# Optimization experiments

Measured on AMD Instinct MI355X. Metric: run time of the kernel, lower is better.

Reference implementation:

```python
import jax, jax.numpy as jnp
import numpy as np

B, S, E, H, V, C = 256, 20, 512, 512, 32000, 1000


def _lstm_step(x, h, c, W, U, b):
    # Keras LSTM, activation='relu', recurrent_activation='sigmoid', gate order i,f,c,o
    z = x @ W + h @ U + b  # (B, 4H)
    i, f, g, o = jnp.split(z, 4, axis=-1)
    i = jax.nn.sigmoid(i)
    f = jax.nn.sigmoid(f)
    g = jax.nn.relu(g)
    o = jax.nn.sigmoid(o)
    c_new = f * c + i * g
    h_new = o * jax.nn.relu(c_new)
    return h_new, c_new


def setup_inputs() -> dict:
    key = jax.random.key(0)
    ks = jax.random.split(key, 24)
    std = 0.05
    d_in1 = S * E + 2 * E  # flattened encoder output + word embed + speaker embed
    inp = {
        "encoded_output": jax.random.normal(ks[0], (B, S, E), jnp.float32),
        "word_embedding": jax.random.normal(ks[1], (B, E), jnp.float32),
        "h0": jax.random.normal(ks[2], (B, H), jnp.float32) * std,
        "c0": jax.random.normal(ks[3], (B, H), jnp.float32) * std,
        "speaker": jax.random.randint(ks[4], (B,), 0, C),
        "addressee": jax.random.randint(ks[5], (B,), 0, C),
        "persona_emb": jax.random.normal(ks[6], (C, E), jnp.float32) * 0.1,
        "W1": jax.random.normal(ks[7], (d_in1, 4 * H), jnp.float32) * std,
        "U1": jax.random.normal(ks[8], (H, 4 * H), jnp.float32) * std,
        "b1": jnp.zeros((4 * H,), jnp.float32),
        "W2": jax.random.normal(ks[9], (H, 4 * H), jnp.float32) * std,
        "U2": jax.random.normal(ks[10], (H, 4 * H), jnp.float32) * std,
        "b2": jnp.zeros((4 * H,), jnp.float32),
        "W3": jax.random.normal(ks[11], (H, 4 * H), jnp.float32) * std,
        "U3": jax.random.normal(ks[12], (H, 4 * H), jnp.float32) * std,
        "b3": jnp.zeros((4 * H,), jnp.float32),
        "W4": jax.random.normal(ks[13], (H, 4 * H), jnp.float32) * std,
        "U4": jax.random.normal(ks[14], (H, 4 * H), jnp.float32) * std,
        "b4": jnp.zeros((4 * H,), jnp.float32),
        "Wd": jax.random.normal(ks[15], (H, V), jnp.float32) * std,
        "bd": jnp.zeros((V,), jnp.float32),
    }
    return inp


def reference(encoded_output, word_embedding, h0, c0, speaker, addressee,
              persona_emb, W1, U1, b1, W2, U2, b2, W3, U3, b3, W4, U4, b4, Wd, bd):
    b = encoded_output.shape[0]
    # The Python double loop in the original is exactly: (B,S,E) -> (B, S*E)
    enc_flat = encoded_output.reshape(b, -1)
    speaker_embed = persona_emb[speaker]  # (B, E)
    # is_speaker=True branch: concat [flattened encoder, word embed, speaker embed]
    x = jnp.concatenate([enc_flat, word_embedding, speaker_embed], axis=-1)
    # seq length is 1, so each LSTM layer is a single cell step;
    # each layer's initial state is the previous layer's final (h, c)
    h1, c1 = _lstm_step(x, h0, c0, W1, U1, b1)
    h2, c2 = _lstm_step(h1, h1, c1, W2, U2, b2)
    h3, c3 = _lstm_step(h2, h2, c2, W3, U3, b3)
    h4, c4 = _lstm_step(h3, h3, c3, W4, U4, b4)
    probs = jax.nn.softmax(h4 @ Wd + bd, axis=-1)  # (B, V)
    return probs, (h4, c4)
```

## Files before the change

### kernel.cpp

```cpp
#include <hip/hip_runtime.h>
#include <cstdint>
#include <cmath>

typedef _Float16 f16;
typedef _Float16 f16x8 __attribute__((ext_vector_type(8)));
typedef float f32x4 __attribute__((ext_vector_type(4)));

__device__ inline void gld_lds16(const void* g, void* l) {
  __builtin_amdgcn_global_load_lds(
      (__attribute__((address_space(1))) void*)(uintptr_t)g,
      (__attribute__((address_space(3))) void*)l, 16, 0, 0);
}

__global__ __launch_bounds__(256) void build_x1_kernel(
    const float* __restrict__ enc, const float* __restrict__ word,
    const float* __restrict__ pers, const int* __restrict__ speaker,
    const float* __restrict__ h0, f16* __restrict__ X)
{
  const int b  = blockIdx.y;
  const int k2 = blockIdx.x * 256 + threadIdx.x;
  const int k  = k2 * 2;
  float v0, v1;
  if (k < 10240) {
    const float* p = enc + (long long)b * 10240 + k; v0 = p[0]; v1 = p[1];
  } else if (k < 10752) {
    const float* p = word + b * 512 + (k - 10240);   v0 = p[0]; v1 = p[1];
  } else if (k < 11264) {
    const float* p = pers + (long long)speaker[b] * 512 + (k - 10752); v0 = p[0]; v1 = p[1];
  } else {
    const float* p = h0 + b * 512 + (k - 11264);     v0 = p[0]; v1 = p[1];
  }
  union { f16 h[2]; unsigned int u; } pk;
  pk.h[0] = (f16)v0; pk.h[1] = (f16)v1;
  ((unsigned int*)X)[(long long)b * 5888 + k2] = pk.u;
}

__global__ __launch_bounds__(256) void wsum_t_kernel(
    const float* __restrict__ W2, const float* __restrict__ U2,
    const float* __restrict__ W3, const float* __restrict__ U3,
    const float* __restrict__ W4, const float* __restrict__ U4,
    f16* __restrict__ out)
{
  const int t = blockIdx.x * 256 + threadIdx.x;
  const int L = blockIdx.y;
  const float* W = (L == 0) ? W2 : (L == 1) ? W3 : W4;
  const float* U = (L == 0) ? U2 : (L == 1) ? U3 : U4;
  const int n  = t & 2047;
  const int k0 = (t >> 11) << 6;
  f16* op = out + (long long)L * (2048 * 512) + (long long)n * 512 + k0;
  for (int kk = 0; kk < 64; kk += 8) {
    f16x8 v;
    #pragma unroll
    for (int j = 0; j < 8; j++) {
      const int k = k0 + kk + j;
      v[j] = (f16)(W[(long long)k * 2048 + n] + U[(long long)k * 2048 + n]);
    }
    *(f16x8*)(op + kk) = v;
  }
}

__global__ __launch_bounds__(256, 2) void gemm_pipe2(
    const f16* __restrict__ A, int lda,
    const float* __restrict__ B0, const float* __restrict__ B1, int ksw, int ldb,
    void* __restrict__ Cv, int ldc, long long c_split_stride, int niter,
    int store_f16)
{
  __shared__ __align__(16) f16 Ah[2][256 * 32];
  __shared__ __align__(16) f16 Bh[2][128 * 40];

  const int tid  = threadIdx.x;
  const int lane = tid & 63;
  const int wave = tid >> 6;
  const int n0 = blockIdx.x * 128;
  const int kbeg = blockIdx.y * (niter * 32);

  const int a_row16 = lane >> 2;
  const int a_ksub  = ((lane & 3) ^ ((lane >> 3) & 3)) * 8;

  const int nl0  = (tid & 63) * 2;
  const int koct = tid >> 6;

  float2 bv[8];

  auto issueB = [&](int kt) {
    const int kb = kbeg + kt * 32 + koct * 8;
    #pragma unroll
    for (int i = 0; i < 8; i++) {
      const int krow = kb + i;
      const float* bp = (krow >= ksw) ? (B1 + (long long)(krow - ksw) * ldb)
                                      : (B0 + (long long)krow * ldb);
      bv[i] = *(const float2*)(bp + n0 + nl0);
    }
  };
  auto issueA = [&](int kt) {
    const int akb = kbeg + kt * 32;
    #pragma unroll
    for (int half = 0; half < 4; half++) {
      const int rb = wave * 64 + half * 16;
      const f16* gp = A + (long long)(rb + a_row16) * lda + akb + a_ksub;
      gld_lds16((const void*)gp, (void*)&Ah[kt & 1][rb * 32]);
    }
  };
  auto writeB = [&](int kt) {
    f16x8 p0, p1;
    #pragma unroll
    for (int i = 0; i < 8; i++) { p0[i] = (f16)bv[i].x; p1[i] = (f16)bv[i].y; }
    *(f16x8*)&Bh[kt & 1][(nl0    ) * 40 + koct * 8] = p0;
    *(f16x8*)&Bh[kt & 1][(nl0 + 1) * 40 + koct * 8] = p1;
  };

  const int wm = (wave & 1) * 128;
  const int wn = (wave >> 1) * 64;
  f32x4 acc[8][4] = {};

  issueB(0); issueA(0); writeB(0);
  __syncthreads();

  for (int kt = 0; kt < niter; kt++) {
    const int buf = kt & 1;
    const bool more = (kt + 1 < niter);
    if (more) { issueB(kt + 1); issueA(kt + 1); }

    f16x8 bf[4];
    #pragma unroll
    for (int ni = 0; ni < 4; ni++) {
      const int n = wn + ni * 16 + (lane & 15);
      bf[ni] = *(const f16x8*)&Bh[buf][n * 40 + (lane >> 4) * 8];
    }
    #pragma unroll
    for (int mi = 0; mi < 8; mi++) {
      const int m = wm + mi * 16 + (lane & 15);
      const f16x8 af = *(const f16x8*)&Ah[buf][m * 32 + (((lane >> 4) ^ ((m >> 1) & 3)) * 8)];
      #pragma unroll
      for (int ni = 0; ni < 4; ni++)
        acc[mi][ni] = __builtin_amdgcn_mfma_f32_16x16x32_f16(af, bf[ni], acc[mi][ni], 0, 0, 0);
    }

    if (more) writeB(kt + 1);
    __syncthreads();
  }

  if (store_f16) {
    f16* Cs = (f16*)Cv + (long long)blockIdx.y * c_split_stride;
    #pragma unroll
    for (int mi = 0; mi < 8; mi++) {
      const int r0 = wm + mi * 16 + (lane >> 4) * 4;
      #pragma unroll
      for (int ni = 0; ni < 4; ni++) {
        const int cc = n0 + wn + ni * 16 + (lane & 15);
        #pragma unroll
        for (int r = 0; r < 4; r++)
          Cs[(long long)(r0 + r) * ldc + cc] = (f16)acc[mi][ni][r];
      }
    }
  } else {
    float* Cs = (float*)Cv + (long long)blockIdx.y * c_split_stride;
    #pragma unroll
    for (int mi = 0; mi < 8; mi++) {
      const int r0 = wm + mi * 16 + (lane >> 4) * 4;
      #pragma unroll
      for (int ni = 0; ni < 4; ni++) {
        const int cc = n0 + wn + ni * 16 + (lane & 15);
        #pragma unroll
        for (int r = 0; r < 4; r++)
          Cs[(long long)(r0 + r) * ldc + cc] = acc[mi][ni][r];
      }
    }
  }
}

__global__ __launch_bounds__(64) void lstm_small_layer(
    const f16* __restrict__ h_in,
    const f16* __restrict__ WsT,
    const float* __restrict__ bias,
    const float* __restrict__ c_prev, float* __restrict__ c_out,
    f16* __restrict__ h16_out, float* __restrict__ h32_out)
{
  const int lane = threadIdx.x;
  const int wid  = blockIdx.x;
  const int jt = wid & 31, mt = wid >> 5;
  const int m0 = mt * 16, j0 = jt * 16;
  const int lj = lane & 15, quad = lane >> 4;

  const f16* Ab = h_in + (long long)(m0 + lj) * 512 + quad * 8;
  const f16* Bb = WsT + (long long)(j0 + lj) * 512 + quad * 8;
  const long long GS = 512LL * 512;

  f32x4 g0 = {}, g1 = {}, g2 = {}, g3 = {};

  f16x8 ca = *(const f16x8*)(Ab);
  f16x8 cb0 = *(const f16x8*)(Bb);
  f16x8 cb1 = *(const f16x8*)(Bb + GS);
  f16x8 cb2 = *(const f16x8*)(Bb + 2 * GS);
  f16x8 cb3 = *(const f16x8*)(Bb + 3 * GS);

  #pragma unroll
  for (int kt = 0; kt < 16; kt++) {
    f16x8 na = ca, nb0 = cb0, nb1 = cb1, nb2 = cb2, nb3 = cb3;
    if (kt < 15) {
      const int k = (kt + 1) * 32;
      na  = *(const f16x8*)(Ab + k);
      nb0 = *(const f16x8*)(Bb + k);
      nb1 = *(const f16x8*)(Bb + GS + k);
      nb2 = *(const f16x8*)(Bb + 2 * GS + k);
      nb3 = *(const f16x8*)(Bb + 3 * GS + k);
    }
    g0 = __builtin_amdgcn_mfma_f32_16x16x32_f16(ca, cb0, g0, 0, 0, 0);
    g1 = __builtin_amdgcn_mfma_f32_16x16x32_f16(ca, cb1, g1, 0, 0, 0);
    g2 = __builtin_amdgcn_mfma_f32_16x16x32_f16(ca, cb2, g2, 0, 0, 0);
    g3 = __builtin_amdgcn_mfma_f32_16x16x32_f16(ca, cb3, g3, 0, 0, 0);
    ca = na; cb0 = nb0; cb1 = nb1; cb2 = nb2; cb3 = nb3;
  }

  const float bi = bias[j0 + lj],        bfv = bias[512 + j0 + lj];
  const float bg = bias[1024 + j0 + lj], bo  = bias[1536 + j0 + lj];
  #pragma unroll
  for (int r = 0; r < 4; r++) {
    const int m = m0 + quad * 4 + r;
    const int idx = m * 512 + j0 + lj;
    const float gi = 1.f / (1.f + expf(-(g0[r] + bi)));
    const float gf = 1.f / (1.f + expf(-(g1[r] + bfv)));
    const float gg = fmaxf(g2[r] + bg, 0.f);
    const float go = 1.f / (1.f + expf(-(g3[r] + bo)));
    const float cn = gf * c_prev[idx] + gi * gg;
    const float hn = go * fmaxf(cn, 0.f);
    c_out[idx] = cn;
    h16_out[idx] = (f16)hn;
    if (h32_out) h32_out[idx] = hn;
  }
}

__global__ __launch_bounds__(256) void gate_kernel(
    const unsigned int* __restrict__ zbase, int nsplit,
    const float* __restrict__ bias,
    const float* __restrict__ c_prev, float* __restrict__ c_out,
    f16* __restrict__ h16_out)
{
  const int idx2 = blockIdx.x * 256 + threadIdx.x;
  const int b  = idx2 >> 8;
  const int j2 = idx2 & 255;
  const int j  = j2 * 2;
  float z[4][2];
  #pragma unroll
  for (int g = 0; g < 4; g++) { z[g][0] = bias[g * 512 + j]; z[g][1] = bias[g * 512 + j + 1]; }
  for (int s = 0; s < nsplit; s++) {
    const unsigned int* zp = zbase + (long long)s * 262144 + b * 1024;
    #pragma unroll
    for (int g = 0; g < 4; g++) {
      union { unsigned int u; f16 h[2]; } v;
      v.u = zp[g * 256 + j2];
      z[g][0] += (float)v.h[0];
      z[g][1] += (float)v.h[1];
    }
  }
  #pragma unroll
  for (int e = 0; e < 2; e++) {
    const float gi = 1.f / (1.f + expf(-z[0][e]));
    const float gf = 1.f / (1.f + expf(-z[1][e]));
    const float gg = fmaxf(z[2][e], 0.f);
    const float go = 1.f / (1.f + expf(-z[3][e]));
    const int idx = b * 512 + j + e;
    const float cn = gf * c_prev[idx] + gi * gg;
    const float hn = go * fmaxf(cn, 0.f);
    c_out[idx] = cn;
    h16_out[idx] = (f16)hn;
  }
}

__global__ __launch_bounds__(1024) void softmax_kernel(
    float* __restrict__ logits, const float* __restrict__ bd)
{
  const int row = blockIdx.x;
  const int t = threadIdx.x;
  float4* rp = (float4*)(logits + (long long)row * 32000);
  const float4* bp = (const float4*)bd;
  float4 l[8];
  float m = -1e30f;
  #pragma unroll
  for (int i = 0; i < 8; i++) {
    const int v = t + i * 1024;
    if (v < 8000) {
      float4 x = rp[v]; const float4 bb = bp[v];
      x.x += bb.x; x.y += bb.y; x.z += bb.z; x.w += bb.w;
      l[i] = x;
      m = fmaxf(m, fmaxf(fmaxf(x.x, x.y), fmaxf(x.z, x.w)));
    } else {
      l[i] = make_float4(-1e30f, -1e30f, -1e30f, -1e30f);
    }
  }
  #pragma unroll
  for (int off = 32; off > 0; off >>= 1) m = fmaxf(m, __shfl_xor(m, off, 64));
  __shared__ float redm[16];
  __shared__ float reds[16];
  const int w = t >> 6;
  if ((t & 63) == 0) redm[w] = m;
  __syncthreads();
  float bm = redm[0];
  #pragma unroll
  for (int i = 1; i < 16; i++) bm = fmaxf(bm, redm[i]);
  float s = 0.f;
  #pragma unroll
  for (int i = 0; i < 8; i++) {
    const float ex = expf(l[i].x - bm), ey = expf(l[i].y - bm);
    const float ez = expf(l[i].z - bm), ew = expf(l[i].w - bm);
    l[i] = make_float4(ex, ey, ez, ew);
    s += (ex + ey) + (ez + ew);
  }
  #pragma unroll
  for (int off = 32; off > 0; off >>= 1) s += __shfl_xor(s, off, 64);
  if ((t & 63) == 0) reds[w] = s;
  __syncthreads();
  float ts = 0.f;
  #pragma unroll
  for (int i = 0; i < 16; i++) ts += reds[i];
  const float inv = 1.0f / ts;
  #pragma unroll
  for (int i = 0; i < 8; i++) {
    const int v = t + i * 1024;
    if (v < 8000) {
      float4 x = l[i];
      x.x *= inv; x.y *= inv; x.z *= inv; x.w *= inv;
      rp[v] = x;
    }
  }
}

extern "C" void kernel_launch(void* const* d_in, const int* in_sizes, int n_in,
                              void* d_out, int out_size, void* d_ws, size_t ws_size,
                              hipStream_t stream) {
  const float* enc     = (const float*)d_in[0];
  const float* word    = (const float*)d_in[1];
  const float* h0      = (const float*)d_in[2];
  const float* c0      = (const float*)d_in[3];
  const int*   speaker = (const int*)d_in[4];
  const float* pers = (const float*)d_in[6];
  const float* W1 = (const float*)d_in[7];
  const float* U1 = (const float*)d_in[8];
  const float* b1 = (const float*)d_in[9];
  const float* W2 = (const float*)d_in[10];
  const float* U2 = (const float*)d_in[11];
  const float* b2 = (const float*)d_in[12];
  const float* W3 = (const float*)d_in[13];
  const float* U3 = (const float*)d_in[14];
  const float* b3 = (const float*)d_in[15];
  const float* W4 = (const float*)d_in[16];
  const float* U4 = (const float*)d_in[17];
  const float* b4 = (const float*)d_in[18];
  const float* Wd = (const float*)d_in[19];
  const float* bd = (const float*)d_in[20];

  float* out = (float*)d_out;
  float* h4_out = out + 8192000;
  float* c4_out = out + 8192000 + 131072;

  f16*   hA   = (f16*)d_ws;
  f16*   hB   = (f16*)((char*)d_ws + 262144);
  f16*   hC   = (f16*)((char*)d_ws + 524288);
  float* cbuf = (float*)((char*)d_ws + 786432);
  f16*   WsT  = (f16*)((char*)d_ws + 2097152);
  f16*   X1h  = (f16*)((char*)d_ws + 8388608);
  f16*   zp16 = (f16*)((char*)d_ws + 16777216);

  const int BIG = 1 << 29;
  const long long LW = 2048LL * 512;

  build_x1_kernel<<<dim3(23, 256), 256, 0, stream>>>(enc, word, pers, speaker, h0, X1h);
  wsum_t_kernel<<<dim3(64, 3), 256, 0, stream>>>(W2, U2, W3, U3, W4, U4, WsT);

  gemm_pipe2<<<dim3(16, 23), 256, 0, stream>>>(
      X1h, 11776, W1, U1, 11264, 2048, zp16, 2048, 524288LL, 16, 1);
  gate_kernel<<<dim3(256), 256, 0, stream>>>((const unsigned int*)zp16, 23, b1, c0, cbuf, hA);

  lstm_small_layer<<<dim3(512), 64, 0, stream>>>(hA, WsT,          b2, cbuf, cbuf, hB, nullptr);
  lstm_small_layer<<<dim3(512), 64, 0, stream>>>(hB, WsT + LW,     b3, cbuf, cbuf, hA, nullptr);
  lstm_small_layer<<<dim3(512), 64, 0, stream>>>(hA, WsT + 2 * LW, b4, cbuf, c4_out, hC, h4_out);

  gemm_pipe2<<<dim3(250, 1), 256, 0, stream>>>(
      hC, 512, Wd, Wd, BIG, 32000, out, 32000, 0LL, 16, 0);

  softmax_kernel<<<dim3(256), 1024, 0, stream>>>(out, bd);
}
```

Before: 335.6 us.

## Deepen GEMM prefetch to three-stage A buffers with explicit vmcnt waits

Measured after the change: 333.3 us. No clear change (-0.7%).

```diff
diff --git a/kernel.cpp b/kernel.cpp
--- a/kernel.cpp
+++ b/kernel.cpp
@@ -11,6 +11,11 @@
       (__attribute__((address_space(1))) void*)(uintptr_t)g,
       (__attribute__((address_space(3))) void*)l, 16, 0, 0);
 }
+
+#define ASM_VMCNT_12() asm volatile("s_waitcnt vmcnt(12)" ::: "memory")
+#define ASM_VMCNT_0()  asm volatile("s_waitcnt vmcnt(0)" ::: "memory")
+#define ASM_LGKM_0()   asm volatile("s_waitcnt lgkmcnt(0)" ::: "memory")
+#define BARRIER() do { __builtin_amdgcn_s_barrier(); asm volatile("" ::: "memory"); } while (0)
 
 __global__ __launch_bounds__(256) void build_x1_kernel(
     const float* __restrict__ enc, const float* __restrict__ word,
@@ -59,13 +64,13 @@
   }
 }
 
-__global__ __launch_bounds__(256, 2) void gemm_pipe2(
+__global__ __launch_bounds__(256, 2) void gemm_pipe3(
     const f16* __restrict__ A, int lda,
     const float* __restrict__ B0, const float* __restrict__ B1, int ksw, int ldb,
     void* __restrict__ Cv, int ldc, long long c_split_stride, int niter,
     int store_f16)
 {
-  __shared__ __align__(16) f16 Ah[2][256 * 32];
+  __shared__ __align__(16) f16 Ah[3][256 * 32];
   __shared__ __align__(16) f16 Bh[2][128 * 40];
 
   const int tid  = threadIdx.x;
@@ -77,12 +82,12 @@
   const int a_row16 = lane >> 2;
   const int a_ksub  = ((lane & 3) ^ ((lane >> 3) & 3)) * 8;
 
-  const int nl0  = (tid & 63) * 2;
+  const int nl0  = lane * 2;
   const int koct = tid >> 6;
 
-  float2 bv[8];
-
-  auto issueB = [&](int kt) {
+  float2 bva[8], bvb[8];
+
+  auto issueB = [&](int kt, float2* bv) {
     const int kb = kbeg + kt * 32 + koct * 8;
     #pragma unroll
     for (int i = 0; i < 8; i++) {
@@ -92,52 +97,80 @@
       bv[i] = *(const float2*)(bp + n0 + nl0);
     }
   };
-  auto issueA = [&](int kt) {
+  auto issueA = [&](int kt, f16* abuf) {
     const int akb = kbeg + kt * 32;
     #pragma unroll
     for (int half = 0; half < 4; half++) {
       const int rb = wave * 64 + half * 16;
       const f16* gp = A + (long long)(rb + a_row16) * lda + akb + a_ksub;
-      gld_lds16((const void*)gp, (void*)&Ah[kt & 1][rb * 32]);
+      gld_lds16((const void*)gp, (void*)&abuf[rb * 32]);
     }
   };
-  auto writeB = [&](int kt) {
+  auto writeB = [&](const float2* bv, f16* bbuf) {
     f16x8 p0, p1;
     #pragma unroll
     for (int i = 0; i < 8; i++) { p0[i] = (f16)bv[i].x; p1[i] = (f16)bv[i].y; }
-    *(f16x8*)&Bh[kt & 1][(nl0    ) * 40 + koct * 8] = p0;
-    *(f16x8*)&Bh[kt & 1][(nl0 + 1) * 40 + koct * 8] = p1;
+    *(f16x8*)&bbuf[(nl0    ) * 40 + koct * 8] = p0;
+    *(f16x8*)&bbuf[(nl0 + 1) * 40 + koct * 8] = p1;
   };
 
   const int wm = (wave & 1) * 128;
   const int wn = (wave >> 1) * 64;
   f32x4 acc[8][4] = {};
 
-  issueB(0); issueA(0); writeB(0);
-  __syncthreads();
-
-  for (int kt = 0; kt < niter; kt++) {
-    const int buf = kt & 1;
-    const bool more = (kt + 1 < niter);
-    if (more) { issueB(kt + 1); issueA(kt + 1); }
-
+  auto compute = [&](const f16* abuf, const f16* bbuf) {
     f16x8 bf[4];
     #pragma unroll
     for (int ni = 0; ni < 4; ni++) {
       const int n = wn + ni * 16 + (lane & 15);
-      bf[ni] = *(const f16x8*)&Bh[buf][n * 40 + (lane >> 4) * 8];
+      bf[ni] = *(const f16x8*)&bbuf[n * 40 + (lane >> 4) * 8];
     }
     #pragma unroll
     for (int mi = 0; mi < 8; mi++) {
       const int m = wm + mi * 16 + (lane & 15);
-      const f16x8 af = *(const f16x8*)&Ah[buf][m * 32 + (((lane >> 4) ^ ((m >> 1) & 3)) * 8)];
+      const f16x8 af = *(const f16x8*)&abuf[m * 32 + (((lane >> 4) ^ ((m >> 1) & 3)) * 8)];
       #pragma unroll
       for (int ni = 0; ni < 4; ni++)
         acc[mi][ni] = __builtin_amdgcn_mfma_f32_16x16x32_f16(af, bf[ni], acc[mi][ni], 0, 0, 0);
     }
-
-    if (more) writeB(kt + 1);
-    __syncthreads();
+  };
+
+  f16* pa_cur  = Ah[0];
+  f16* pa_nxt  = Ah[1];
+  f16* pa_free = Ah[2];
+
+  issueB(0, bva); issueA(0, pa_cur);
+  issueB(1, bvb); issueA(1, pa_nxt);
+  ASM_VMCNT_12();
+  writeB(bva, Bh[0]);
+  ASM_LGKM_0();
+  BARRIER();
+
+  for (int kt = 0; kt < niter; kt += 2) {
+    {
+      const bool iss = (kt + 2 < niter);
+      if (iss) { issueB(kt + 2, bva); issueA(kt + 2, pa_free); }
+      compute(pa_cur, Bh[0]);
+      if (kt + 1 < niter) {
+        if (iss) { ASM_VMCNT_12(); } else { ASM_VMCNT_0(); }
+        writeB(bvb, Bh[1]);
+      }
+      ASM_LGKM_0();
+      BARRIER();
+      f16* t = pa_cur; pa_cur = pa_nxt; pa_nxt = pa_free; pa_free = t;
+    }
+    if (kt + 1 < niter) {
+      const bool iss = (kt + 3 < niter);
+      if (iss) { issueB(kt + 3, bvb); issueA(kt + 3, pa_free); }
+      compute(pa_cur, Bh[1]);
+      if (kt + 2 < niter) {
+        if (iss) { ASM_VMCNT_12(); } else { ASM_VMCNT_0(); }
+        writeB(bva, Bh[0]);
+      }
+      ASM_LGKM_0();
+      BARRIER();
+      f16* t = pa_cur; pa_cur = pa_nxt; pa_nxt = pa_free; pa_free = t;
+    }
   }
 
   if (store_f16) {
@@ -367,7 +400,7 @@
   build_x1_kernel<<<dim3(23, 256), 256, 0, stream>>>(enc, word, pers, speaker, h0, X1h);
   wsum_t_kernel<<<dim3(64, 3), 256, 0, stream>>>(W2, U2, W3, U3, W4, U4, WsT);
 
-  gemm_pipe2<<<dim3(16, 23), 256, 0, stream>>>(
+  gemm_pipe3<<<dim3(16, 23), 256, 0, stream>>>(
       X1h, 11776, W1, U1, 11264, 2048, zp16, 2048, 524288LL, 16, 1);
   gate_kernel<<<dim3(256), 256, 0, stream>>>((const unsigned int*)zp16, 23, b1, c0, cbuf, hA);
 
@@ -375,7 +408,7 @@
   lstm_small_layer<<<dim3(512), 64, 0, stream>>>(hB, WsT + LW,     b3, cbuf, cbuf, hA, nullptr);
   lstm_small_layer<<<dim3(512), 64, 0, stream>>>(hA, WsT + 2 * LW, b4, cbuf, c4_out, hC, h4_out);
 
-  gemm_pipe2<<<dim3(250, 1), 256, 0, stream>>>(
+  gemm_pipe3<<<dim3(250, 1), 256, 0, stream>>>(
       hC, 512, Wd, Wd, BIG, 32000, out, 32000, 0LL, 16, 0);
 
   softmax_kernel<<<dim3(256), 1024, 0, stream>>>(out, bd);
```

## Replace LDS-staged GEMM with register-streamed single-wave GEMM and more blocks

Applied to the files above, without the earlier changes.

New measurement: 389.0 us. 1.16x slower.

```diff
diff --git a/kernel.cpp b/kernel.cpp
--- a/kernel.cpp
+++ b/kernel.cpp
@@ -5,12 +5,6 @@
 typedef _Float16 f16;
 typedef _Float16 f16x8 __attribute__((ext_vector_type(8)));
 typedef float f32x4 __attribute__((ext_vector_type(4)));
-
-__device__ inline void gld_lds16(const void* g, void* l) {
-  __builtin_amdgcn_global_load_lds(
-      (__attribute__((address_space(1))) void*)(uintptr_t)g,
-      (__attribute__((address_space(3))) void*)l, 16, 0, 0);
-}
 
 __global__ __launch_bounds__(256) void build_x1_kernel(
     const float* __restrict__ enc, const float* __restrict__ word,
@@ -59,113 +53,91 @@
   }
 }
 
-__global__ __launch_bounds__(256, 2) void gemm_pipe2(
+template<int NITER>
+__global__ __launch_bounds__(64) void gemm_stream(
     const f16* __restrict__ A, int lda,
     const float* __restrict__ B0, const float* __restrict__ B1, int ksw, int ldb,
-    void* __restrict__ Cv, int ldc, long long c_split_stride, int niter,
+    void* __restrict__ Cv, int ldc, long long c_split_stride,
     int store_f16)
 {
-  __shared__ __align__(16) f16 Ah[2][256 * 32];
-  __shared__ __align__(16) f16 Bh[2][128 * 40];
-
-  const int tid  = threadIdx.x;
-  const int lane = tid & 63;
-  const int wave = tid >> 6;
-  const int n0 = blockIdx.x * 128;
-  const int kbeg = blockIdx.y * (niter * 32);
-
-  const int a_row16 = lane >> 2;
-  const int a_ksub  = ((lane & 3) ^ ((lane >> 3) & 3)) * 8;
-
-  const int nl0  = (tid & 63) * 2;
-  const int koct = tid >> 6;
-
-  float2 bv[8];
-
-  auto issueB = [&](int kt) {
-    const int kb = kbeg + kt * 32 + koct * 8;
-    #pragma unroll
-    for (int i = 0; i < 8; i++) {
-      const int krow = kb + i;
-      const float* bp = (krow >= ksw) ? (B1 + (long long)(krow - ksw) * ldb)
-                                      : (B0 + (long long)krow * ldb);
-      bv[i] = *(const float2*)(bp + n0 + nl0);
-    }
+  const int lane = threadIdx.x;
+  const int lj = lane & 15, lh = lane >> 4;
+  const int mt    = blockIdx.x;
+  const int nt    = blockIdx.y;
+  const int split = blockIdx.z;
+  const int n0 = nt * 32;
+  const int m0 = mt * 128;
+  const int k0 = split * (NITER * 32);
+
+  const f16* Abase = A + (long long)(m0 + lj) * lda + k0 + lh * 8;
+  const long long arow16 = (long long)16 * lda;
+
+  auto loadA = [&](int kk, f16x8* fr) {
+    #pragma unroll
+    for (int mi = 0; mi < 8; mi++)
+      fr[mi] = *(const f16x8*)(Abase + mi * arow16 + kk);
   };
-  auto issueA = [&](int kt) {
-    const int akb = kbeg + kt * 32;
-    #pragma unroll
-    for (int half = 0; half < 4; half++) {
-      const int rb = wave * 64 + half * 16;
-      const f16* gp = A + (long long)(rb + a_row16) * lda + akb + a_ksub;
-      gld_lds16((const void*)gp, (void*)&Ah[kt & 1][rb * 32]);
+  auto loadB = [&](int kk, float* b0v, float* b1v) {
+    const int kb = k0 + kk + lh * 8;
+    const float* bp = (kb >= ksw) ? (B1 + (long long)(kb - ksw) * ldb)
+                                  : (B0 + (long long)kb * ldb);
+    bp += n0 + lj;
+    #pragma unroll
+    for (int j = 0; j < 8; j++) {
+      b0v[j] = bp[(long long)j * ldb];
+      b1v[j] = bp[(long long)j * ldb + 16];
     }
   };
-  auto writeB = [&](int kt) {
-    f16x8 p0, p1;
-    #pragma unroll
-    for (int i = 0; i < 8; i++) { p0[i] = (f16)bv[i].x; p1[i] = (f16)bv[i].y; }
-    *(f16x8*)&Bh[kt & 1][(nl0    ) * 40 + koct * 8] = p0;
-    *(f16x8*)&Bh[kt & 1][(nl0 + 1) * 40 + koct * 8] = p1;
-  };
-
-  const int wm = (wave & 1) * 128;
-  const int wn = (wave >> 1) * 64;
-  f32x4 acc[8][4] = {};
-
-  issueB(0); issueA(0); writeB(0);
-  __syncthreads();
-
-  for (int kt = 0; kt < niter; kt++) {
-    const int buf = kt & 1;
-    const bool more = (kt + 1 < niter);
-    if (more) { issueB(kt + 1); issueA(kt + 1); }
-
-    f16x8 bf[4];
-    #pragma unroll
-    for (int ni = 0; ni < 4; ni++) {
-      const int n = wn + ni * 16 + (lane & 15);
-      bf[ni] = *(const f16x8*)&Bh[buf][n * 40 + (lane >> 4) * 8];
-    }
+
+  f32x4 acc[8][2] = {};
+  f16x8 aC[8], aN[8];
+  float b0C[8], b1C[8], b0N[8], b1N[8];
+
+  loadA(0, aC);
+  loadB(0, b0C, b1C);
+
+  #pragma unroll
+  for (int kt = 0; kt < NITER; kt++) {
+    if (kt + 1 < NITER) {
+      loadA((kt + 1) * 32, aN);
+      loadB((kt + 1) * 32, b0N, b1N);
+    }
+    f16x8 bf0, bf1;
+    #pragma unroll
+    for (int j = 0; j < 8; j++) { bf0[j] = (f16)b0C[j]; bf1[j] = (f16)b1C[j]; }
     #pragma unroll
     for (int mi = 0; mi < 8; mi++) {
-      const int m = wm + mi * 16 + (lane & 15);
-      const f16x8 af = *(const f16x8*)&Ah[buf][m * 32 + (((lane >> 4) ^ ((m >> 1) & 3)) * 8)];
+      acc[mi][0] = __builtin_amdgcn_mfma_f32_16x16x32_f16(aC[mi], bf0, acc[mi][0], 0, 0, 0);
+      acc[mi][1] = __builtin_amdgcn_mfma_f32_16x16x32_f16(aC[mi], bf1, acc[mi][1], 0, 0, 0);
+    }
+    if (kt + 1 < NITER) {
       #pragma unroll
-      for (int ni = 0; ni < 4; ni++)
-        acc[mi][ni] = __builtin_amdgcn_mfma_f32_16x16x32_f16(af, bf[ni], acc[mi][ni], 0, 0, 0);
-    }
-
-    if (more) writeB(kt + 1);
-    __syncthreads();
+      for (int mi = 0; mi < 8; mi++) aC[mi] = aN[mi];
+      #pragma unroll
+      for (int j = 0; j < 8; j++) { b0C[j] = b0N[j]; b1C[j] = b1N[j]; }
+    }
   }
 
   if (store_f16) {
-    f16* Cs = (f16*)Cv + (long long)blockIdx.y * c_split_stride;
-    #pragma unroll
-    for (int mi = 0; mi < 8; mi++) {
-      const int r0 = wm + mi * 16 + (lane >> 4) * 4;
+    f16* Cs = (f16*)Cv + (long long)split * c_split_stride;
+    #pragma unroll
+    for (int mi = 0; mi < 8; mi++)
       #pragma unroll
-      for (int ni = 0; ni < 4; ni++) {
-        const int cc = n0 + wn + ni * 16 + (lane & 15);
+      for (int ni = 0; ni < 2; ni++)
         #pragma unroll
         for (int r = 0; r < 4; r++)
-          Cs[(long long)(r0 + r) * ldc + cc] = (f16)acc[mi][ni][r];
-      }
-    }
+          Cs[(long long)(m0 + mi * 16 + lh * 4 + r) * ldc + n0 + ni * 16 + lj] =
+              (f16)acc[mi][ni][r];
   } else {
-    float* Cs = (float*)Cv + (long long)blockIdx.y * c_split_stride;
-    #pragma unroll
-    for (int mi = 0; mi < 8; mi++) {
-      const int r0 = wm + mi * 16 + (lane >> 4) * 4;
+    float* Cs = (float*)Cv + (long long)split * c_split_stride;
+    #pragma unroll
+    for (int mi = 0; mi < 8; mi++)
       #pragma unroll
-      for (int ni = 0; ni < 4; ni++) {
-        const int cc = n0 + wn + ni * 16 + (lane & 15);
+      for (int ni = 0; ni < 2; ni++)
         #pragma unroll
         for (int r = 0; r < 4; r++)
-          Cs[(long long)(r0 + r) * ldc + cc] = acc[mi][ni][r];
-      }
-    }
+          Cs[(long long)(m0 + mi * 16 + lh * 4 + r) * ldc + n0 + ni * 16 + lj] =
+              acc[mi][ni][r];
   }
 }
 
@@ -367,16 +339,16 @@
   build_x1_kernel<<<dim3(23, 256), 256, 0, stream>>>(enc, word, pers, speaker, h0, X1h);
   wsum_t_kernel<<<dim3(64, 3), 256, 0, stream>>>(W2, U2, W3, U3, W4, U4, WsT);
 
-  gemm_pipe2<<<dim3(16, 23), 256, 0, stream>>>(
-      X1h, 11776, W1, U1, 11264, 2048, zp16, 2048, 524288LL, 16, 1);
-  gate_kernel<<<dim3(256), 256, 0, stream>>>((const unsigned int*)zp16, 23, b1, c0, cbuf, hA);
+  gemm_stream<23><<<dim3(2, 64, 16), 64, 0, stream>>>(
+      X1h, 11776, W1, U1, 11264, 2048, zp16, 2048, 524288LL, 1);
+  gate_kernel<<<dim3(256), 256, 0, stream>>>((const unsigned int*)zp16, 16, b1, c0, cbuf, hA);
 
   lstm_small_layer<<<dim3(512), 64, 0, stream>>>(hA, WsT,          b2, cbuf, cbuf, hB, nullptr);
   lstm_small_layer<<<dim3(512), 64, 0, stream>>>(hB, WsT + LW,     b3, cbuf, cbuf, hA, nullptr);
   lstm_small_layer<<<dim3(512), 64, 0, stream>>>(hA, WsT + 2 * LW, b4, cbuf, c4_out, hC, h4_out);
 
-  gemm_pipe2<<<dim3(250, 1), 256, 0, stream>>>(
-      hC, 512, Wd, Wd, BIG, 32000, out, 32000, 0LL, 16, 0);
+  gemm_stream<16><<<dim3(2, 1000, 1), 64, 0, stream>>>(
+      hC, 512, Wd, Wd, BIG, 32000, out, 32000, 0LL, 0);
 
   softmax_kernel<<<dim3(256), 1024, 0, stream>>>(out, bd);
 }
```
